# Performance work log

Hardware: AMD Instinct MI355X
Metric: run time of the kernel (lower is better)

Reference implementation:

```python
import jax, jax.numpy as jnp
import numpy as np

L, D, T, B = 4, 256, 4096, 8  # n_layer, hidden, seq_len, batch


def setup_inputs() -> dict:
    key = jax.random.key(0)
    ks = jax.random.split(key, 12)
    x = jax.random.normal(ks[0], (B, T, D), dtype=jnp.float32)
    # stable LRU diagonal init: |lambda| in [0.9, 0.999], phase in [0, pi/10]
    r = jax.random.uniform(ks[1], (L, D), minval=0.9, maxval=0.999)
    nu_log = jnp.log(-jnp.log(r))
    theta = jax.random.uniform(ks[2], (L, D), minval=1e-4, maxval=np.pi / 10)
    theta_log = jnp.log(theta)
    gamma_log = 0.5 * jnp.log(1.0 - r ** 2)  # normalization gamma = sqrt(1-|lam|^2)
    s = 0.02  # matches truncated_normal_init std
    B_re = s * jax.random.normal(ks[3], (L, D, D), dtype=jnp.float32)
    B_im = s * jax.random.normal(ks[4], (L, D, D), dtype=jnp.float32)
    C_re = s * jax.random.normal(ks[5], (L, D, D), dtype=jnp.float32)
    C_im = s * jax.random.normal(ks[6], (L, D, D), dtype=jnp.float32)
    D_vec = s * jax.random.normal(ks[7], (L, D), dtype=jnp.float32)
    Wg = s * jax.random.normal(ks[8], (L, D, D), dtype=jnp.float32)
    ln_scale = jnp.ones((L, D), dtype=jnp.float32)
    ln_bias = jnp.zeros((L, D), dtype=jnp.float32)
    return dict(x=x, nu_log=nu_log, theta_log=theta_log, gamma_log=gamma_log,
                B_re=B_re, B_im=B_im, C_re=C_re, C_im=C_im, D_vec=D_vec,
                Wg=Wg, ln_scale=ln_scale, ln_bias=ln_bias)


def _layer_norm(x, scale, bias):
    mu = x.mean(-1, keepdims=True)
    var = x.var(-1, keepdims=True)
    return (x - mu) / jnp.sqrt(var + 1e-5) * scale + bias


def _lru_scan(lam, bu):
    # lam: (D,) complex diagonal transition; bu: (T,B,D) complex inputs
    a = jnp.broadcast_to(lam, bu.shape)

    def comb(e1, e2):
        a1, b1 = e1
        a2, b2 = e2
        return a1 * a2, a2 * b1 + b2

    _, h = jax.lax.associative_scan(comb, (a, bu), axis=0)
    return h  # (T,B,D) complex


def reference(x, nu_log, theta_log, gamma_log, B_re, B_im, C_re, C_im, D_vec, Wg, ln_scale, ln_bias):
    u = jnp.transpose(x, (1, 0, 2))  # time-major (T,B,D), mirrors torch permute(1,0,2)
    for l in range(L):  # fixed small layer loop
        z = _layer_norm(u, ln_scale[l], ln_bias[l])
        lam = jnp.exp(-jnp.exp(nu_log[l]) + 1j * jnp.exp(theta_log[l]))  # (D,)
        Bm = B_re[l] + 1j * B_im[l]
        bu = jnp.einsum('tbd,ed->tbe', z.astype(jnp.complex64), Bm) * jnp.exp(gamma_log[l])
        h = _lru_scan(lam, bu)  # (T,B,D) complex state (h0 = 0, matching get_zero_internal_state)
        y = jnp.einsum('tbe,de->tbd', h, C_re[l] + 1j * C_im[l]).real + D_vec[l] * z
        y = y * jax.nn.sigmoid(jnp.einsum('tbd,ed->tbe', z, Wg[l]))  # gating=True output gate
        u = u + y  # residual
    return jnp.transpose(u, (1, 0, 2))  # back to (B,T,D)
```

## Files before the change

kernel.cpp:

```cpp
#include <hip/hip_runtime.h>
#include <hip/hip_bf16.h>

#define NLAYER 4
#define DDIM 256
#define TSEQ 4096
#define NBATCH 8
#define MROWS (NBATCH * TSEQ)
#define CLEN 32
#define NCHUNK (TSEQ / CLEN)

typedef float f32x4 __attribute__((ext_vector_type(4)));
typedef short bf16x8 __attribute__((ext_vector_type(8)));

__device__ __forceinline__ float bf2f(unsigned short u) {
    union { unsigned int i; float f; } v; v.i = ((unsigned int)u) << 16; return v.f;
}
__device__ __forceinline__ unsigned short f2bf(float f) {
    union { float f; unsigned int i; } v; v.f = f;
    unsigned int r = v.i + 0x7fffu + ((v.i >> 16) & 1u);
    return (unsigned short)(r >> 16);
}

__device__ __forceinline__ void gload16(const unsigned short* g, unsigned short* l) {
    __builtin_amdgcn_global_load_lds(
        (const __attribute__((address_space(1))) unsigned int*)g,
        (__attribute__((address_space(3))) unsigned int*)l, 16, 0, 0);
}

__global__ __launch_bounds__(256) void prepack_kernel(
    const float* __restrict__ nu_log, const float* __restrict__ theta_log,
    const float* __restrict__ gamma_log,
    const float* __restrict__ B_re, const float* __restrict__ B_im,
    const float* __restrict__ C_re, const float* __restrict__ C_im,
    const float* __restrict__ Wg,
    unsigned short* __restrict__ wBre, unsigned short* __restrict__ wBim,
    unsigned short* __restrict__ wWg, unsigned short* __restrict__ wCre,
    unsigned short* __restrict__ wCimn,
    float* __restrict__ lam_re, float* __restrict__ lam_im,
    float* __restrict__ lamC_re, float* __restrict__ lamC_im)
{
    int idx = blockIdx.x * 256 + threadIdx.x;
    const int total = NLAYER * DDIM * DDIM;
    if (idx < total) {
        int l = idx >> 16;
        int e = (idx >> 8) & 255;
        float gam = expf(gamma_log[l * DDIM + e]);
        wBre[idx]  = f2bf(B_re[idx] * gam);
        wBim[idx]  = f2bf(B_im[idx] * gam);
        wWg[idx]   = f2bf(Wg[idx]);
        wCre[idx]  = f2bf(C_re[idx]);
        wCimn[idx] = f2bf(-C_im[idx]);
    }
    if (idx < NLAYER * DDIM) {
        float mag = expf(-expf(nu_log[idx]));
        float th  = expf(theta_log[idx]);
        float ar = mag * cosf(th);
        float ai = mag * sinf(th);
        lam_re[idx] = ar;
        lam_im[idx] = ai;
        #pragma unroll
        for (int s = 0; s < 5; ++s) {
            float nr = ar * ar - ai * ai;
            float ni = 2.0f * ar * ai;
            ar = nr; ai = ni;
        }
        lamC_re[idx] = ar;
        lamC_im[idx] = ai;
    }
}

__global__ __launch_bounds__(256) void ln_kernel(
    const float* __restrict__ u, unsigned short* __restrict__ z,
    const float* __restrict__ scale, const float* __restrict__ bias,
    float2* __restrict__ rowStats)
{
    int wid = threadIdx.x >> 6;
    int lane = threadIdx.x & 63;
    int row = blockIdx.x * 4 + wid;
    const float4 v = *reinterpret_cast<const float4*>(u + (size_t)row * DDIM + lane * 4);
    float s  = v.x + v.y + v.z + v.w;
    float s2 = v.x * v.x + v.y * v.y + v.z * v.z + v.w * v.w;
    #pragma unroll
    for (int off = 32; off > 0; off >>= 1) {
        s  += __shfl_xor(s, off);
        s2 += __shfl_xor(s2, off);
    }
    float mu  = s * (1.0f / DDIM);
    float var = s2 * (1.0f / DDIM) - mu * mu;
    float inv = rsqrtf(var + 1e-5f);
    if (lane == 0) { float2 st; st.x = mu; st.y = inv; rowStats[row] = st; }
    float zv[4] = { v.x, v.y, v.z, v.w };
    ushort4 o;
    unsigned short* op = (unsigned short*)&o;
    #pragma unroll
    for (int j = 0; j < 4; ++j) {
        int d = lane * 4 + j;
        op[j] = f2bf((zv[j] - mu) * inv * scale[d] + bias[d]);
    }
    *reinterpret_cast<ushort4*>(z + (size_t)row * DDIM + lane * 4) = o;
}

__global__ __launch_bounds__(256) void gemm1_kernel(
    const unsigned short* __restrict__ z,
    const unsigned short* __restrict__ wBre, const unsigned short* __restrict__ wBim,
    const unsigned short* __restrict__ wWg,
    unsigned short* __restrict__ bure, unsigned short* __restrict__ buim,
    unsigned short* __restrict__ sg,
    const float* __restrict__ lam_re, const float* __restrict__ lam_im,
    float2* __restrict__ fin)
{
    const int m0 = blockIdx.x * 128;
    const int n0 = blockIdx.y * 64;

    __shared__ unsigned short Al[128 * 64];
    __shared__ unsigned short Wl[3][64 * 64];

    const int tid = threadIdx.x;
    const int lane = tid & 63;
    const int wid = tid >> 6;
    const int wr = wid >> 1, wc = wid & 1;
    const int lr = lane >> 3;
    const int lc = lane & 7;

    f32x4 acc[3][4][2] = {};

    for (int ko = 0; ko < 256; ko += 64) {
        #pragma unroll
        for (int it = 0; it < 4; ++it) {
            int s = wid * 4 + it;
            int r = s * 8 + lr;
            int gc = lc ^ (r & 7);
            gload16(z + (size_t)(m0 + r) * 256 + ko + gc * 8, &Al[s * 512]);
        }
        #pragma unroll
        for (int it = 0; it < 2; ++it) {
            int s = wid * 2 + it;
            int r = s * 8 + lr;
            int gc = lc ^ (r & 7);
            size_t off = (size_t)(n0 + r) * 256 + ko + gc * 8;
            gload16(wBre + off, &Wl[0][s * 512]);
            gload16(wBim + off, &Wl[1][s * 512]);
            gload16(wWg  + off, &Wl[2][s * 512]);
        }
        __syncthreads();

        #pragma unroll
        for (int k2 = 0; k2 < 64; k2 += 32) {
            int ac = (k2 >> 3) + (lane >> 4);
            bf16x8 a[4];
            #pragma unroll
            for (int mi = 0; mi < 4; ++mi) {
                int ar = wr * 64 + mi * 16 + (lane & 15);
                a[mi] = *reinterpret_cast<const bf16x8*>(&Al[ar * 64 + ((ac ^ (ar & 7)) * 8)]);
            }
            int br0 = wc * 32 + (lane & 15);
            int br1 = br0 + 16;
            #pragma unroll
            for (int mat = 0; mat < 3; ++mat) {
                bf16x8 b0 = *reinterpret_cast<const bf16x8*>(&Wl[mat][br0 * 64 + ((ac ^ (br0 & 7)) * 8)]);
                bf16x8 b1 = *reinterpret_cast<const bf16x8*>(&Wl[mat][br1 * 64 + ((ac ^ (br1 & 7)) * 8)]);
                #pragma unroll
                for (int mi = 0; mi < 4; ++mi) {
                    acc[mat][mi][0] = __builtin_amdgcn_mfma_f32_16x16x32_bf16(a[mi], b0, acc[mat][mi][0], 0, 0, 0);
                    acc[mat][mi][1] = __builtin_amdgcn_mfma_f32_16x16x32_bf16(a[mi], b1, acc[mat][mi][1], 0, 0, 0);
                }
            }
        }
        __syncthreads();
    }

    unsigned short* Tre = Al;
    unsigned short* Tim = &Wl[0][0];
    #pragma unroll
    for (int mat = 0; mat < 3; ++mat) {
        unsigned short* out = (mat == 0) ? bure : ((mat == 1) ? buim : sg);
        #pragma unroll
        for (int mi = 0; mi < 4; ++mi) {
            #pragma unroll
            for (int ni = 0; ni < 2; ++ni) {
                int cl = wc * 32 + ni * 16 + (lane & 15);
                int rl = wr * 64 + mi * 16 + (lane >> 4) * 4;
                #pragma unroll
                for (int j = 0; j < 4; ++j) {
                    float v = acc[mat][mi][ni][j];
                    unsigned short bv;
                    if (mat == 2) { bv = f2bf(1.0f / (1.0f + expf(-v))); }
                    else          { bv = f2bf(v); }
                    out[(size_t)(m0 + rl + j) * 256 + n0 + cl] = bv;
                    if (mat == 0) Tre[(rl + j) * 64 + cl] = bv;
                    if (mat == 1) Tim[(rl + j) * 64 + cl] = bv;
                }
            }
        }
    }
    __syncthreads();
    {
        const int c = tid >> 6;
        const int col = tid & 63;
        const int dglob = n0 + col;
        const float lr_ = lam_re[dglob], li_ = lam_im[dglob];
        float hr = 0.0f, hi = 0.0f;
        #pragma unroll 8
        for (int k = 0; k < CLEN; ++k) {
            int row = c * 32 + k;
            float br = bf2f(Tre[row * 64 + col]);
            float bi = bf2f(Tim[row * 64 + col]);
            float nr = fmaf(lr_, hr, fmaf(-li_, hi, br));
            float ni = fmaf(lr_, hi, fmaf(li_, hr, bi));
            hr = nr; hi = ni;
        }
        const int b = m0 >> 12;
        const int cglob = ((m0 & 4095) >> 5) + c;
        float2 o; o.x = hr; o.y = hi;
        fin[((size_t)b * 256 + dglob) * 128 + cglob] = o;
    }
}

__global__ __launch_bounds__(256) void scan_prefix_kernel(
    const float2* __restrict__ fin, float2* __restrict__ pre,
    const float* __restrict__ lamC_re, const float* __restrict__ lamC_im)
{
    const int lane = threadIdx.x & 63;
    const int w = blockIdx.x * 4 + (threadIdx.x >> 6);
    const int d = w & 255;
    const float ar = lamC_re[d], ai = lamC_im[d];
    const float4 f = *reinterpret_cast<const float4*>(fin + (size_t)w * 128 + lane * 2);
    const float f0r = f.x, f0i = f.y, f1r = f.z, f1i = f.w;
    float Tr = fmaf(ar, f0r, fmaf(-ai, f0i, f1r));
    float Ti = fmaf(ar, f0i, fmaf(ai, f0r, f1i));
    float Ar_ = ar * ar - ai * ai;
    float Ai_ = 2.0f * ar * ai;
    #pragma unroll
    for (int s = 1; s < 64; s <<= 1) {
        float ur = __shfl_up(Tr, s, 64);
        float ui = __shfl_up(Ti, s, 64);
        if (lane >= s) {
            Tr = fmaf(Ar_, ur, fmaf(-Ai_, ui, Tr));
            Ti = fmaf(Ar_, ui, fmaf(Ai_, ur, Ti));
        }
        float nr = Ar_ * Ar_ - Ai_ * Ai_;
        float ni = 2.0f * Ar_ * Ai_;
        Ar_ = nr; Ai_ = ni;
    }
    float Er = __shfl_up(Tr, 1, 64);
    float Ei = __shfl_up(Ti, 1, 64);
    if (lane == 0) { Er = 0.0f; Ei = 0.0f; }
    float P1r = fmaf(ar, Er, fmaf(-ai, Ei, f0r));
    float P1i = fmaf(ar, Ei, fmaf(ai, Er, f0i));
    float4 o; o.x = Er; o.y = Ei; o.z = P1r; o.w = P1i;
    *reinterpret_cast<float4*>(pre + (size_t)w * 128 + lane * 2) = o;
}

__global__ __launch_bounds__(256) void gemm2_kernel(
    const unsigned short* __restrict__ bure, const unsigned short* __restrict__ buim,
    const unsigned short* __restrict__ wCre, const unsigned short* __restrict__ wCimn,
    const unsigned short* __restrict__ sg, const float2* __restrict__ pre,
    const float* __restrict__ lam_re, const float* __restrict__ lam_im,
    const float* __restrict__ scale, const float* __restrict__ bias,
    const float2* __restrict__ rowStats,
    const float* __restrict__ Dv, const float* __restrict__ uin, float* __restrict__ uout,
    const float* __restrict__ nscale, const float* __restrict__ nbias,
    unsigned short* __restrict__ zout, float2* __restrict__ statsOut, int writeLN)
{
    const int m0 = blockIdx.x * 64;

    __shared__ unsigned short Ar[64 * 64];
    __shared__ unsigned short Ai[64 * 64];
    __shared__ unsigned short Cr[256 * 64];
    __shared__ unsigned short Ci[256 * 64];

    const int tid = threadIdx.x;
    const int lane = tid & 63;
    const int wid = tid >> 6;
    const int lr = lane >> 3;
    const int lc = lane & 7;

    const int b = m0 >> 12;
    const int cbase = (m0 & 4095) >> 5;

    f32x4 acc[4][4] = {};

    for (int ko = 0; ko < 256; ko += 64) {
        #pragma unroll
        for (int it = 0; it < 8; ++it) {
            int s = wid * 8 + it;
            int r = s * 8 + lr;
            int gc = lc ^ (r & 7);
            size_t off = (size_t)r * 256 + ko + gc * 8;
            gload16(wCre + off, &Cr[s * 512]);
            gload16(wCimn + off, &Ci[s * 512]);
        }

        if (tid < 128) {
            const int c = tid >> 6;
            const int dl = tid & 63;
            const int dg = ko + dl;
            const float lre = lam_re[dg], lim = lam_im[dg];
            float2 p = pre[((size_t)b * 256 + dg) * 128 + cbase + c];
            unsigned short vre[CLEN], vim[CLEN];
            size_t gbase = (size_t)(m0 + c * 32) * 256 + dg;
            #pragma unroll
            for (int k = 0; k < CLEN; ++k) {
                vre[k] = bure[gbase + (size_t)k * 256];
                vim[k] = buim[gbase + (size_t)k * 256];
            }
            float hr = p.x, hi = p.y;
            #pragma unroll
            for (int k = 0; k < CLEN; ++k) {
                float br = bf2f(vre[k]);
                float bi = bf2f(vim[k]);
                float nr = fmaf(lre, hr, fmaf(-lim, hi, br));
                float ni = fmaf(lre, hi, fmaf(lim, hr, bi));
                hr = nr; hi = ni;
                int row = c * 32 + k;
                int off = row * 64 + (((dl >> 3) ^ (row & 7)) * 8) + (dl & 7);
                Ar[off] = f2bf(nr);
                Ai[off] = f2bf(ni);
            }
        }
        __syncthreads();

        #pragma unroll
        for (int k2 = 0; k2 < 64; k2 += 32) {
            int ac = (k2 >> 3) + (lane >> 4);
            bf16x8 are[4], aim[4];
            #pragma unroll
            for (int mi = 0; mi < 4; ++mi) {
                int arow = mi * 16 + (lane & 15);
                int idx = arow * 64 + ((ac ^ (arow & 7)) * 8);
                are[mi] = *reinterpret_cast<const bf16x8*>(&Ar[idx]);
                aim[mi] = *reinterpret_cast<const bf16x8*>(&Ai[idx]);
            }
            #pragma unroll
            for (int ni = 0; ni < 4; ++ni) {
                int brow = wid * 64 + ni * 16 + (lane & 15);
                int ib = brow * 64 + ((ac ^ (brow & 7)) * 8);
                bf16x8 bre = *reinterpret_cast<const bf16x8*>(&Cr[ib]);
                bf16x8 bim = *reinterpret_cast<const bf16x8*>(&Ci[ib]);
                #pragma unroll
                for (int mi = 0; mi < 4; ++mi) {
                    acc[mi][ni] = __builtin_amdgcn_mfma_f32_16x16x32_bf16(are[mi], bre, acc[mi][ni], 0, 0, 0);
                    acc[mi][ni] = __builtin_amdgcn_mfma_f32_16x16x32_bf16(aim[mi], bim, acc[mi][ni], 0, 0, 0);
                }
            }
        }
        __syncthreads();
    }

    float uvals[4][4][4];
    float rs[4][4], rs2[4][4];
    #pragma unroll
    for (int mi = 0; mi < 4; ++mi)
        #pragma unroll
        for (int j = 0; j < 4; ++j) { rs[mi][j] = 0.0f; rs2[mi][j] = 0.0f; }

    #pragma unroll
    for (int mi = 0; mi < 4; ++mi) {
        #pragma unroll
        for (int ni = 0; ni < 4; ++ni) {
            int col = wid * 64 + ni * 16 + (lane & 15);
            int mrow = m0 + mi * 16 + (lane >> 4) * 4;
            float dv = Dv[col];
            float scc = scale[col], bcc = bias[col];
            #pragma unroll
            for (int j = 0; j < 4; ++j) {
                size_t idx = (size_t)(mrow + j) * 256 + col;
                float2 st = rowStats[mrow + j];
                float uv = uin[idx];
                float zz = (uv - st.x) * st.y * scc + bcc;
                float s = bf2f(sg[idx]);
                float o = uv + (acc[mi][ni][j] + dv * zz) * s;
                uout[idx] = o;
                uvals[mi][ni][j] = o;
                rs[mi][j] += o;
                rs2[mi][j] += o * o;
            }
        }
    }

    if (writeLN) {
        #pragma unroll
        for (int mi = 0; mi < 4; ++mi)
            #pragma unroll
            for (int j = 0; j < 4; ++j)
                #pragma unroll
                for (int off = 1; off < 16; off <<= 1) {
                    rs[mi][j]  += __shfl_xor(rs[mi][j], off);
                    rs2[mi][j] += __shfl_xor(rs2[mi][j], off);
                }
        float* sS   = (float*)Ar;
        float* sS2  = sS + 256;
        float* sMu  = sS2 + 256;
        float* sInv = sMu + 64;
        __syncthreads();
        if ((lane & 15) == 0) {
            int hi = lane >> 4;
            #pragma unroll
            for (int mi = 0; mi < 4; ++mi)
                #pragma unroll
                for (int j = 0; j < 4; ++j) {
                    int row = mi * 16 + hi * 4 + j;
                    sS[wid * 64 + row]  = rs[mi][j];
                    sS2[wid * 64 + row] = rs2[mi][j];
                }
        }
        __syncthreads();
        if (tid < 64) {
            float s  = sS[tid] + sS[64 + tid] + sS[128 + tid] + sS[192 + tid];
            float s2 = sS2[tid] + sS2[64 + tid] + sS2[128 + tid] + sS2[192 + tid];
            float mu  = s * (1.0f / 256.0f);
            float var = s2 * (1.0f / 256.0f) - mu * mu;
            float inv = rsqrtf(var + 1e-5f);
            sMu[tid] = mu; sInv[tid] = inv;
            float2 st; st.x = mu; st.y = inv;
            statsOut[m0 + tid] = st;
        }
        __syncthreads();
        #pragma unroll
        for (int mi = 0; mi < 4; ++mi) {
            #pragma unroll
            for (int ni = 0; ni < 4; ++ni) {
                int col = wid * 64 + ni * 16 + (lane & 15);
                float nsc = nscale[col], nbi = nbias[col];
                #pragma unroll
                for (int j = 0; j < 4; ++j) {
                    int row = mi * 16 + (lane >> 4) * 4 + j;
                    float zz = (uvals[mi][ni][j] - sMu[row]) * sInv[row] * nsc + nbi;
                    zout[(size_t)(m0 + row) * 256 + col] = f2bf(zz);
                }
            }
        }
    }
}

extern "C" void kernel_launch(void* const* d_in, const int* in_sizes, int n_in,
                              void* d_out, int out_size, void* d_ws, size_t ws_size,
                              hipStream_t stream) {
    const float* x         = (const float*)d_in[0];
    const float* nu_log    = (const float*)d_in[1];
    const float* theta_log = (const float*)d_in[2];
    const float* gamma_log = (const float*)d_in[3];
    const float* B_re      = (const float*)d_in[4];
    const float* B_im      = (const float*)d_in[5];
    const float* C_re      = (const float*)d_in[6];
    const float* C_im      = (const float*)d_in[7];
    const float* D_vec     = (const float*)d_in[8];
    const float* Wg        = (const float*)d_in[9];
    const float* ln_scale  = (const float*)d_in[10];
    const float* ln_bias   = (const float*)d_in[11];
    float* out = (float*)d_out;

    const size_t MSZ = (size_t)MROWS * DDIM;
    const size_t WSZ = (size_t)NLAYER * DDIM * DDIM;
    const size_t FSZ = (size_t)NBATCH * DDIM * NCHUNK;

    unsigned short* b16 = (unsigned short*)d_ws;
    unsigned short* z     = b16;
    unsigned short* sg    = b16 + MSZ;
    unsigned short* bure  = b16 + 2 * MSZ;
    unsigned short* buim  = b16 + 3 * MSZ;
    unsigned short* wBre  = b16 + 4 * MSZ;
    unsigned short* wBim  = wBre + WSZ;
    unsigned short* wWg   = wBim + WSZ;
    unsigned short* wCre  = wWg + WSZ;
    unsigned short* wCimn = wCre + WSZ;
    float* lam_re  = (float*)(wCimn + WSZ);
    float* lam_im  = lam_re + NLAYER * DDIM;
    float* lamC_re = lam_im + NLAYER * DDIM;
    float* lamC_im = lamC_re + NLAYER * DDIM;
    float2* fin = (float2*)(lamC_im + NLAYER * DDIM);
    float2* pre = fin + FSZ;
    float2* statsA = pre + FSZ;
    float2* statsB = statsA + MROWS;

    prepack_kernel<<<1024, 256, 0, stream>>>(nu_log, theta_log, gamma_log,
                                             B_re, B_im, C_re, C_im, Wg,
                                             wBre, wBim, wWg, wCre, wCimn,
                                             lam_re, lam_im, lamC_re, lamC_im);

    ln_kernel<<<MROWS / 4, 256, 0, stream>>>(x, z, ln_scale, ln_bias, statsA);

    for (int l = 0; l < NLAYER; ++l) {
        const float* uin = (l == 0) ? x : out;
        const float* lre = lam_re + l * DDIM;
        const float* lim = lam_im + l * DDIM;
        float2* statsIn  = (l & 1) ? statsB : statsA;
        float2* statsOut = (l & 1) ? statsA : statsB;
        int nl = (l < NLAYER - 1) ? (l + 1) : l;
        gemm1_kernel<<<dim3(MROWS / 128, 4), 256, 0, stream>>>(
            z, wBre + l * DDIM * DDIM, wBim + l * DDIM * DDIM, wWg + l * DDIM * DDIM,
            bure, buim, sg, lre, lim, fin);
        scan_prefix_kernel<<<512, 256, 0, stream>>>(fin, pre,
                                                    lamC_re + l * DDIM, lamC_im + l * DDIM);
        gemm2_kernel<<<MROWS / 64, 256, 0, stream>>>(
            bure, buim, wCre + l * DDIM * DDIM, wCimn + l * DDIM * DDIM,
            sg, pre, lre, lim,
            ln_scale + l * DDIM, ln_bias + l * DDIM, statsIn,
            D_vec + l * DDIM, uin, out,
            ln_scale + nl * DDIM, ln_bias + nl * DDIM,
            z, statsOut, (l < NLAYER - 1) ? 1 : 0);
    }
}
```

Baseline: 275.1 us.

## Interleave bu real/imag storage and prefetch next scan chunk in gemm2

gemm1 now writes the real and imaginary bf16 parts of bu packed into one 32-bit word, so gemm2's scan threads fetch both with a single load instead of two. gemm2 hoists the pre-state loads and double-buffers the bu loads in registers, issuing the next K-slice's loads before the current chain and waiting with hand-written waitcnt/barrier instead of __syncthreads. The uvals register array is dropped and the LN pass re-reads uout from global memory to cut register pressure. Risks are 64 extra VGPRs for the two buffers, fragile manual waitcnt ordering, and an extra global read in the LN pass.

```diff
diff --git a/kernel.cpp b/kernel.cpp
--- a/kernel.cpp
+++ b/kernel.cpp
@@ -104,8 +104,7 @@
     const unsigned short* __restrict__ z,
     const unsigned short* __restrict__ wBre, const unsigned short* __restrict__ wBim,
     const unsigned short* __restrict__ wWg,
-    unsigned short* __restrict__ bure, unsigned short* __restrict__ buim,
-    unsigned short* __restrict__ sg,
+    unsigned int* __restrict__ buri, unsigned short* __restrict__ sg,
     const float* __restrict__ lam_re, const float* __restrict__ lam_im,
     float2* __restrict__ fin)
 {
@@ -172,24 +171,20 @@
     unsigned short* Tre = Al;
     unsigned short* Tim = &Wl[0][0];
     #pragma unroll
-    for (int mat = 0; mat < 3; ++mat) {
-        unsigned short* out = (mat == 0) ? bure : ((mat == 1) ? buim : sg);
-        #pragma unroll
-        for (int mi = 0; mi < 4; ++mi) {
-            #pragma unroll
-            for (int ni = 0; ni < 2; ++ni) {
-                int cl = wc * 32 + ni * 16 + (lane & 15);
-                int rl = wr * 64 + mi * 16 + (lane >> 4) * 4;
-                #pragma unroll
-                for (int j = 0; j < 4; ++j) {
-                    float v = acc[mat][mi][ni][j];
-                    unsigned short bv;
-                    if (mat == 2) { bv = f2bf(1.0f / (1.0f + expf(-v))); }
-                    else          { bv = f2bf(v); }
-                    out[(size_t)(m0 + rl + j) * 256 + n0 + cl] = bv;
-                    if (mat == 0) Tre[(rl + j) * 64 + cl] = bv;
-                    if (mat == 1) Tim[(rl + j) * 64 + cl] = bv;
-                }
+    for (int mi = 0; mi < 4; ++mi) {
+        #pragma unroll
+        for (int ni = 0; ni < 2; ++ni) {
+            int cl = wc * 32 + ni * 16 + (lane & 15);
+            int rl = wr * 64 + mi * 16 + (lane >> 4) * 4;
+            #pragma unroll
+            for (int j = 0; j < 4; ++j) {
+                unsigned short br = f2bf(acc[0][mi][ni][j]);
+                unsigned short bi = f2bf(acc[1][mi][ni][j]);
+                buri[(size_t)(m0 + rl + j) * 256 + n0 + cl] = ((unsigned int)bi << 16) | br;
+                Tre[(rl + j) * 64 + cl] = br;
+                Tim[(rl + j) * 64 + cl] = bi;
+                float g = acc[2][mi][ni][j];
+                sg[(size_t)(m0 + rl + j) * 256 + n0 + cl] = f2bf(1.0f / (1.0f + expf(-g)));
             }
         }
     }
@@ -251,8 +246,36 @@
     *reinterpret_cast<float4*>(pre + (size_t)w * 128 + lane * 2) = o;
 }
 
+#define G2_LOAD_BU(dst, koff)                                              \
+    {                                                                      \
+        size_t gb = (size_t)(m0 + sc * 32) * 256 + (koff) + dl;            \
+        _Pragma("unroll")                                                  \
+        for (int k = 0; k < CLEN; ++k)                                     \
+            dst[k] = buri[gb + (size_t)k * 256];                           \
+    }
+
+#define G2_CHAIN(src, kk)                                                  \
+    {                                                                      \
+        const int dg = kk * 64 + dl;                                       \
+        const float lre = lam_re[dg], lim = lam_im[dg];                    \
+        float hr = pre4[kk].x, hi = pre4[kk].y;                            \
+        _Pragma("unroll")                                                  \
+        for (int k = 0; k < CLEN; ++k) {                                   \
+            unsigned int v = src[k];                                       \
+            float br = bf2f((unsigned short)(v & 0xffffu));                \
+            float bi = bf2f((unsigned short)(v >> 16));                    \
+            float nr = fmaf(lre, hr, fmaf(-lim, hi, br));                  \
+            float ni = fmaf(lre, hi, fmaf(lim, hr, bi));                   \
+            hr = nr; hi = ni;                                              \
+            int row = sc * 32 + k;                                         \
+            int off = row * 64 + (((dl >> 3) ^ (row & 7)) * 8) + (dl & 7); \
+            Ar[off] = f2bf(nr);                                            \
+            Ai[off] = f2bf(ni);                                            \
+        }                                                                  \
+    }
+
 __global__ __launch_bounds__(256) void gemm2_kernel(
-    const unsigned short* __restrict__ bure, const unsigned short* __restrict__ buim,
+    const unsigned int* __restrict__ buri,
     const unsigned short* __restrict__ wCre, const unsigned short* __restrict__ wCimn,
     const unsigned short* __restrict__ sg, const float2* __restrict__ pre,
     const float* __restrict__ lam_re, const float* __restrict__ lam_im,
@@ -277,10 +300,24 @@
 
     const int b = m0 >> 12;
     const int cbase = (m0 & 4095) >> 5;
+    const bool isScan = (tid < 128);
+    const int sc = tid >> 6;
+    const int dl = tid & 63;
 
     f32x4 acc[4][4] = {};
 
-    for (int ko = 0; ko < 256; ko += 64) {
+    float2 pre4[4];
+    unsigned int vbuA[CLEN], vbuB[CLEN];
+    if (isScan) {
+        #pragma unroll
+        for (int kk = 0; kk < 4; ++kk)
+            pre4[kk] = pre[((size_t)b * 256 + kk * 64 + dl) * 128 + cbase + sc];
+        G2_LOAD_BU(vbuA, 0)
+    }
+
+    #pragma unroll
+    for (int kk = 0; kk < 4; ++kk) {
+        const int ko = kk * 64;
         #pragma unroll
         for (int it = 0; it < 8; ++it) {
             int s = wid * 8 + it;
@@ -290,35 +327,26 @@
             gload16(wCre + off, &Cr[s * 512]);
             gload16(wCimn + off, &Ci[s * 512]);
         }
-
-        if (tid < 128) {
-            const int c = tid >> 6;
-            const int dl = tid & 63;
-            const int dg = ko + dl;
-            const float lre = lam_re[dg], lim = lam_im[dg];
-            float2 p = pre[((size_t)b * 256 + dg) * 128 + cbase + c];
-            unsigned short vre[CLEN], vim[CLEN];
-            size_t gbase = (size_t)(m0 + c * 32) * 256 + dg;
-            #pragma unroll
-            for (int k = 0; k < CLEN; ++k) {
-                vre[k] = bure[gbase + (size_t)k * 256];
-                vim[k] = buim[gbase + (size_t)k * 256];
-            }
-            float hr = p.x, hi = p.y;
-            #pragma unroll
-            for (int k = 0; k < CLEN; ++k) {
-                float br = bf2f(vre[k]);
-                float bi = bf2f(vim[k]);
-                float nr = fmaf(lre, hr, fmaf(-lim, hi, br));
-                float ni = fmaf(lre, hi, fmaf(lim, hr, bi));
-                hr = nr; hi = ni;
-                int row = c * 32 + k;
-                int off = row * 64 + (((dl >> 3) ^ (row & 7)) * 8) + (dl & 7);
-                Ar[off] = f2bf(nr);
-                Ai[off] = f2bf(ni);
-            }
-        }
-        __syncthreads();
+        asm volatile("" ::: "memory");
+
+        if (isScan) {
+            if ((kk & 1) == 0) {
+                G2_CHAIN(vbuA, kk)
+                if (kk < 3) G2_LOAD_BU(vbuB, ko + 64)
+            } else {
+                G2_CHAIN(vbuB, kk)
+                if (kk < 3) G2_LOAD_BU(vbuA, ko + 64)
+            }
+        }
+
+        if (isScan) {
+            if (kk < 3) asm volatile("s_waitcnt vmcnt(32) lgkmcnt(0)" ::: "memory");
+            else        asm volatile("s_waitcnt vmcnt(0) lgkmcnt(0)" ::: "memory");
+        } else {
+            asm volatile("s_waitcnt vmcnt(0)" ::: "memory");
+        }
+        __builtin_amdgcn_s_barrier();
+        __builtin_amdgcn_sched_barrier(0);
 
         #pragma unroll
         for (int k2 = 0; k2 < 64; k2 += 32) {
@@ -344,10 +372,10 @@
                 }
             }
         }
-        __syncthreads();
-    }
-
-    float uvals[4][4][4];
+        asm volatile("s_waitcnt lgkmcnt(0)" ::: "memory");
+        __builtin_amdgcn_s_barrier();
+    }
+
     float rs[4][4], rs2[4][4];
     #pragma unroll
     for (int mi = 0; mi < 4; ++mi)
@@ -371,7 +399,6 @@
                 float s = bf2f(sg[idx]);
                 float o = uv + (acc[mi][ni][j] + dv * zz) * s;
                 uout[idx] = o;
-                uvals[mi][ni][j] = o;
                 rs[mi][j] += o;
                 rs2[mi][j] += o * o;
             }
@@ -425,8 +452,10 @@
                 #pragma unroll
                 for (int j = 0; j < 4; ++j) {
                     int row = mi * 16 + (lane >> 4) * 4 + j;
-                    float zz = (uvals[mi][ni][j] - sMu[row]) * sInv[row] * nsc + nbi;
-                    zout[(size_t)(m0 + row) * 256 + col] = f2bf(zz);
+                    size_t idx = (size_t)(m0 + row) * 256 + col;
+                    float o = uout[idx];
+                    float zz = (o - sMu[row]) * sInv[row] * nsc + nbi;
+                    zout[idx] = f2bf(zz);
                 }
             }
         }
@@ -457,8 +486,7 @@
     unsigned short* b16 = (unsigned short*)d_ws;
     unsigned short* z     = b16;
     unsigned short* sg    = b16 + MSZ;
-    unsigned short* bure  = b16 + 2 * MSZ;
-    unsigned short* buim  = b16 + 3 * MSZ;
+    unsigned int*   buri  = (unsigned int*)(b16 + 2 * MSZ);
     unsigned short* wBre  = b16 + 4 * MSZ;
     unsigned short* wBim  = wBre + WSZ;
     unsigned short* wWg   = wBim + WSZ;
@@ -489,11 +517,11 @@
         int nl = (l < NLAYER - 1) ? (l + 1) : l;
         gemm1_kernel<<<dim3(MROWS / 128, 4), 256, 0, stream>>>(
             z, wBre + l * DDIM * DDIM, wBim + l * DDIM * DDIM, wWg + l * DDIM * DDIM,
-            bure, buim, sg, lre, lim, fin);
+            buri, sg, lre, lim, fin);
         scan_prefix_kernel<<<512, 256, 0, stream>>>(fin, pre,
                                                     lamC_re + l * DDIM, lamC_im + l * DDIM);
         gemm2_kernel<<<MROWS / 64, 256, 0, stream>>>(
-            bure, buim, wCre + l * DDIM * DDIM, wCimn + l * DDIM * DDIM,
+            buri, wCre + l * DDIM * DDIM, wCimn + l * DDIM * DDIM,
             sg, pre, lre, lim,
             ln_scale + l * DDIM, ln_bias + l * DDIM, statsIn,
             D_vec + l * DDIM, uin, out,
```

New measurement: 349.5 us, median of 2. 27.0% more time.
